# Kernel tuning notes

Measured on AMD Instinct MI355X. Metric: run time of the kernel, lower is better.

The kernel has to match this reference:

```python
import jax, jax.numpy as jnp
import numpy as np

B, H, W, C = 16, 48, 48, 256
D_INNER = 2 * C          # ssm_ratio = 2.0
D_STATE = 1
DT_RANK = C // 16        # mamba convention: dt_rank = d_model // 16
HID = 4 * C              # mlp_ratio = 4.0
N = H * W


def _grid_neighbors(h, w):
    idx = np.arange(h * w).reshape(h, w)
    pad_r = -np.ones((1, w), np.int64)
    pad_c = -np.ones((h, 1), np.int64)
    up = np.concatenate([pad_r, idx[:-1]], 0)
    down = np.concatenate([idx[1:], pad_r], 0)
    left = np.concatenate([pad_c, idx[:, :-1]], 1)
    right = np.concatenate([idx[:, 1:], pad_c], 1)
    nb = np.stack([up, down, left, right], -1).reshape(h * w, 4)
    valid = nb >= 0
    return jnp.asarray(np.where(valid, nb, 0), np.int32), jnp.asarray(valid)

_NBR, _VALID = _grid_neighbors(H, W)


def _mst(x):
    """Input-adaptive MST (Prim) on the 4-connected pixel grid.
    Edge weight = exp(1 - cosine_similarity) between adjacent pixel features.
    Returns (order, par): Prim insertion order (a valid BFS-like topological order:
    every node's parent appears earlier) and parent node id per node."""
    b = x.shape[0]
    f = x.reshape(b, N, C)
    f = f / (jnp.linalg.norm(f, axis=-1, keepdims=True) + 1e-8)
    cos = jnp.einsum('bnc,bnkc->bnk', f, f[:, _NBR])          # (B,N,4)
    wgt = jnp.where(_VALID, jnp.exp(1.0 - cos), jnp.inf)

    def prim(wb):
        key = jnp.full((N,), jnp.inf, wb.dtype).at[0].set(0.0)
        par = jnp.zeros((N,), jnp.int32)
        intree = jnp.zeros((N,), bool)

        def step(carry, _):
            key, par, intree = carry
            u = jnp.argmin(jnp.where(intree, jnp.inf, key)).astype(jnp.int32)
            intree = intree.at[u].set(True)
            nb, wv = _NBR[u], wb[u]
            better = (~intree[nb]) & (wv < key[nb])
            key = key.at[nb].set(jnp.where(better, wv, key[nb]))
            par = par.at[nb].set(jnp.where(better, u, par[nb]))
            return (key, par, intree), u

        (_, par, _), order = jax.lax.scan(step, (key, par, intree), None, length=N)
        return order, par

    return jax.vmap(prim)(wgt)


def _ln(x, g, b):
    m = jnp.mean(x, -1, keepdims=True)
    v = jnp.var(x, -1, keepdims=True)
    return (x - m) * jax.lax.rsqrt(v + 1e-5) * g + b


def _tree_ssm(xn, order, par, W_in, b_in, W_xp, W_dt, b_dt, A_log, Dp, W_out, b_out):
    """Mamba-style selective scan generalized to a tree: the hidden state of node v
    recurses from its MST parent instead of the previous sequence position."""
    b = xn.shape[0]
    xf = xn.reshape(b, N, C)
    xz = xf @ W_in + b_in                               # (B,N,2*D_INNER)
    xi, z = xz[..., :D_INNER], xz[..., D_INNER:]
    xi = jax.nn.silu(xi)
    dbc = xi @ W_xp                                     # (B,N,DT_RANK+2)
    dtr = dbc[..., :DT_RANK]
    Bv = dbc[..., DT_RANK:DT_RANK + 1]                  # d_state = 1
    Cv = dbc[..., DT_RANK + 1:DT_RANK + 2]
    dt = jax.nn.softplus(dtr @ W_dt + b_dt)             # (B,N,D_INNER)
    A = -jnp.exp(A_log)                                 # (D_INNER,)
    decay = jnp.exp(dt * A)
    Bx = dt * Bv * xi

    def tree_scan(ob, pb, db, xb):
        def step(hbuf, v):
            hv = db[v] * hbuf[pb[v]] + xb[v]            # h[v] = decay*h[parent] + B*x
            return hbuf.at[v].set(hv), None
        hbuf, _ = jax.lax.scan(step, jnp.zeros((N, D_INNER), db.dtype), ob)
        return hbuf

    h = jax.vmap(tree_scan)(order, par, decay, Bx)      # (B,N,D_INNER)
    y = Cv * h + Dp * xi
    return ((y * jax.nn.silu(z)) @ W_out + b_out).reshape(xn.shape)


def setup_inputs():
    key = jax.random.key(0)
    ks = jax.random.split(key, 8)
    g = lambda k, shp, s=0.02: jax.random.normal(k, shp, jnp.float32) * s
    return {
        "x": jax.random.normal(ks[0], (B, H, W, C), jnp.float32),
        "norm1_w": jnp.ones((C,), jnp.float32), "norm1_b": jnp.zeros((C,), jnp.float32),
        "norm2_w": jnp.ones((C,), jnp.float32), "norm2_b": jnp.zeros((C,), jnp.float32),
        "W_in": g(ks[1], (C, 2 * D_INNER)), "b_in": jnp.zeros((2 * D_INNER,), jnp.float32),
        "W_xp": g(ks[2], (D_INNER, DT_RANK + 2 * D_STATE)),
        "W_dt": g(ks[3], (DT_RANK, D_INNER), 0.1), "b_dt": jnp.full((D_INNER,), -2.0, jnp.float32),
        "A_log": jnp.zeros((D_INNER,), jnp.float32), "Dp": jnp.ones((D_INNER,), jnp.float32),
        "W_out": g(ks[4], (D_INNER, C)), "b_out": jnp.zeros((C,), jnp.float32),
        "fc1_w": g(ks[5], (C, HID)), "fc1_b": jnp.zeros((HID,), jnp.float32),
        "fc2_w": g(ks[6], (HID, C)), "fc2_b": jnp.zeros((C,), jnp.float32),
    }


def reference(x, norm1_w, norm1_b, norm2_w, norm2_b, W_in, b_in, W_xp, W_dt, b_dt,
              A_log, Dp, W_out, b_out, fc1_w, fc1_b, fc2_w, fc2_b):
    order, par = _mst(jax.lax.stop_gradient(x))         # torch.no_grad() MST
    x = x + _tree_ssm(_ln(x, norm1_w, norm1_b), order, par,
                      W_in, b_in, W_xp, W_dt, b_dt, A_log, Dp, W_out, b_out)
    h = jax.nn.gelu(_ln(x, norm2_w, norm2_b) @ fc1_w + fc1_b, approximate=False)
    return x + h @ fc2_w + fc2_b
```

## Files before the change

### kernel.cpp

```cpp
#include <hip/hip_runtime.h>
#include <math.h>

#define NN 2304
#define BB 16
#define CC 256
#define DI 512
#define MM (BB*NN)

typedef __attribute__((ext_vector_type(8))) short bf16x8;
typedef __attribute__((ext_vector_type(4))) float f32x4;

__device__ inline unsigned short f2b(float f){
  unsigned u = __float_as_uint(f);
  u = u + 0x7FFFu + ((u>>16)&1u);
  return (unsigned short)(u>>16);
}
__device__ inline float b2f(unsigned short s){ return __uint_as_float(((unsigned)s)<<16); }

__global__ __launch_bounds__(256) void k_wconv(const float* __restrict__ in, unsigned short* __restrict__ out, int R, int Ccols){
  int idx = blockIdx.x*256 + threadIdx.x;
  if (idx >= R*Ccols) return;
  int r = idx / Ccols, c = idx - r*Ccols;
  out[(size_t)c*R + r] = f2b(in[idx]);
}
__global__ __launch_bounds__(256) void k_t32(const float* __restrict__ in, float* __restrict__ out, int R, int Ccols){
  int idx = blockIdx.x*256 + threadIdx.x;
  if (idx >= R*Ccols) return;
  int r = idx / Ccols, c = idx - r*Ccols;
  out[(size_t)c*R + r] = in[idx];
}

__global__ __launch_bounds__(256) void k_norm(const float* __restrict__ x, float* __restrict__ innorm){
  int row = blockIdx.x*4 + (threadIdx.x>>6); int lane = threadIdx.x&63;
  float4 v = *(const float4*)(x + (size_t)row*CC + lane*4);
  float s = v.x*v.x + v.y*v.y + v.z*v.z + v.w*v.w;
  #pragma unroll
  for (int o=32;o;o>>=1) s += __shfl_xor(s,o);
  if (lane==0) innorm[row] = 1.0f/(sqrtf(s)+1e-8f);
}

__global__ __launch_bounds__(256) void k_edge(const float* __restrict__ x, const float* __restrict__ innorm, float* __restrict__ wgt){
  int g = blockIdx.x*4 + (threadIdx.x>>6); int lane = threadIdx.x&63;
  int b = g/NN, n = g - b*NN;
  int r = n/48, c = n - (n/48)*48;
  const float* xb = x + ((size_t)b*NN)*CC;
  float4 vu = *(const float4*)(xb + (size_t)n*CC + lane*4);
  int nb0=(r>0)?n-48:-1, nb1=(r<47)?n+48:-1, nb2=(c>0)?n-1:-1, nb3=(c<47)?n+1:-1;
  float d0=0,d1=0,d2=0,d3=0;
  if (nb0>=0){ float4 t=*(const float4*)(xb+(size_t)nb0*CC+lane*4); d0=vu.x*t.x+vu.y*t.y+vu.z*t.z+vu.w*t.w; }
  if (nb1>=0){ float4 t=*(const float4*)(xb+(size_t)nb1*CC+lane*4); d1=vu.x*t.x+vu.y*t.y+vu.z*t.z+vu.w*t.w; }
  if (nb2>=0){ float4 t=*(const float4*)(xb+(size_t)nb2*CC+lane*4); d2=vu.x*t.x+vu.y*t.y+vu.z*t.z+vu.w*t.w; }
  if (nb3>=0){ float4 t=*(const float4*)(xb+(size_t)nb3*CC+lane*4); d3=vu.x*t.x+vu.y*t.y+vu.z*t.z+vu.w*t.w; }
  #pragma unroll
  for (int o=32;o;o>>=1){ d0+=__shfl_xor(d0,o); d1+=__shfl_xor(d1,o); d2+=__shfl_xor(d2,o); d3+=__shfl_xor(d3,o); }
  if (lane==0){
    float inu = innorm[g];
    float inf_ = __uint_as_float(0x7F800000u);
    float4 w;
    w.x = (nb0>=0)? expf(1.0f - d0*(inu*innorm[g-n+nb0])) : inf_;
    w.y = (nb1>=0)? expf(1.0f - d1*(inu*innorm[g-n+nb1])) : inf_;
    w.z = (nb2>=0)? expf(1.0f - d2*(inu*innorm[g-n+nb2])) : inf_;
    w.w = (nb3>=0)? expf(1.0f - d3*(inu*innorm[g-n+nb3])) : inf_;
    *(float4*)(wgt + (size_t)g*4) = w;
  }
}

#define INFB 0x7F800000u
__device__ void mst_body(unsigned char* smem, const float* __restrict__ wgt, int b,
    unsigned short* __restrict__ parpos_g, int* __restrict__ lvlorder,
    int* __restrict__ lvlstart, int* __restrict__ nlvl)
{
  unsigned* comp   = (unsigned*)smem;
  unsigned* bestw  = (unsigned*)(smem + 9216);
  unsigned* bestid = (unsigned*)(smem + 18432);
  unsigned* tmask  = (unsigned*)(smem + 27648);
  unsigned* parpd  = (unsigned*)(smem + 36864);
  unsigned short* fr0 = (unsigned short*)(smem + 46080);
  unsigned short* fr1 = (unsigned short*)(smem + 50688);
  int* ctr = (int*)(smem + 55296);
  const int tid = threadIdx.x;
  const float* wb = wgt + (size_t)b*NN*4;

  #pragma unroll
  for (int k=0;k<9;k++){ int v=tid+k*256; comp[v]=v; tmask[v]=0u; }
  __syncthreads();

  for (int round=0; round<14; round++){
    #pragma unroll
    for (int k=0;k<9;k++){ int v=tid+k*256; bestw[v]=INFB; bestid[v]=0xFFFFFFFFu; }
    __syncthreads();
    unsigned candw[9], candi[9];
    #pragma unroll
    for (int k=0;k<9;k++){
      int v=tid+k*256;
      unsigned cv=comp[v];
      int r=v/48, c=v-(v/48)*48;
      float4 w4 = *(const float4*)(wb + (size_t)v*4);
      unsigned cw=INFB, ci=0xFFFFFFFFu;
      if (r>0  && comp[v-48]!=cv){ unsigned wv=__float_as_uint(w4.x); if (wv<cw){cw=wv;ci=(unsigned)(v*4+0);} }
      if (r<47 && comp[v+48]!=cv){ unsigned wv=__float_as_uint(w4.y); if (wv<cw){cw=wv;ci=(unsigned)(v*4+1);} }
      if (c>0  && comp[v-1] !=cv){ unsigned wv=__float_as_uint(w4.z); if (wv<cw){cw=wv;ci=(unsigned)(v*4+2);} }
      if (c<47 && comp[v+1] !=cv){ unsigned wv=__float_as_uint(w4.w); if (wv<cw){cw=wv;ci=(unsigned)(v*4+3);} }
      candw[k]=cw; candi[k]=ci;
      if (cw!=INFB) atomicMin(&bestw[cv], cw);
    }
    __syncthreads();
    #pragma unroll
    for (int k=0;k<9;k++){
      if (candw[k]!=INFB){
        int v=tid+k*256; unsigned cv=comp[v];
        if (bestw[cv]==candw[k]) atomicMin(&bestid[cv], candi[k]);
      }
    }
    __syncthreads();
    unsigned hookS[9];
    #pragma unroll
    for (int k=0;k<9;k++){
      int v=tid+k*256; hookS[k]=0xFFFFFFFFu;
      if (comp[v]!=(unsigned)v) continue;
      unsigned id=bestid[v];
      if (id==0xFFFFFFFFu) continue;
      int u=(int)(id>>2), d=(int)(id&3);
      int o = u + ((d==0)?-48:(d==1)?48:(d==2)?-1:1);
      unsigned s = comp[o];
      unsigned sid = bestid[s];
      bool mutual=false;
      if (sid!=0xFFFFFFFFu){
        int su=(int)(sid>>2), sd=(int)(sid&3);
        int so = su + ((sd==0)?-48:(sd==1)?48:(sd==2)?-1:1);
        mutual = (comp[so]==(unsigned)v);
      }
      if (!mutual || (unsigned)v>s) hookS[k]=s;
    }
    __syncthreads();
    #pragma unroll
    for (int k=0;k<9;k++){
      if (hookS[k]==0xFFFFFFFFu) continue;
      int v=tid+k*256;
      unsigned id=bestid[v];
      int u=(int)(id>>2), d=(int)(id&3);
      int o = u + ((d==0)?-48:(d==1)?48:(d==2)?-1:1);
      comp[v]=hookS[k];
      atomicOr(&tmask[u], 1u<<d);
      atomicOr(&tmask[o], 1u<<(d^1));
    }
    __syncthreads();
    for (int it=0; it<16; it++){
      if (tid==0) ctr[1]=0;
      __syncthreads();
      int ch=0;
      #pragma unroll
      for (int k=0;k<9;k++){
        int v=tid+k*256;
        unsigned c1=comp[v], c2=comp[c1];
        if (c1!=c2){ comp[v]=c2; ch=1; }
      }
      if (ch) atomicAdd(&ctr[1],1);
      __syncthreads();
      if (ctr[1]==0) break;
    }
    if (tid==0) ctr[2]=0;
    __syncthreads();
    int rc=0;
    #pragma unroll
    for (int k=0;k<9;k++){ int v=tid+k*256; if (comp[v]==(unsigned)v) rc++; }
    if (rc) atomicAdd(&ctr[2], rc);
    __syncthreads();
    if (ctr[2]<=1) break;
  }
  #pragma unroll
  for (int k=0;k<9;k++){ int v=tid+k*256; parpd[v]=0xFFFFFFFFu; }
  __syncthreads();
  if (tid >= 64) return;

  volatile unsigned* vpar = parpd;
  volatile int* vctr = ctr;
  volatile unsigned short* vf0 = fr0;
  volatile unsigned short* vf1 = fr1;
  if (tid==0){
    vpar[0]=0u; vf0[0]=0;
    lvlstart[b*(NN+2)+0]=0;
    lvlorder[b*NN+0]=0;
    parpos_g[b*NN+0]=0;
  }
  __builtin_amdgcn_wave_barrier();
  __builtin_amdgcn_sched_barrier(0);
  int lvl=0, base=0, cnt=1;
  volatile unsigned short* frA=vf0;
  volatile unsigned short* frB=vf1;
  while (true){
    if (tid==0) vctr[0]=0;
    __builtin_amdgcn_wave_barrier();
    __builtin_amdgcn_sched_barrier(0);
    for (int i=tid;i<cnt;i+=64){
      int v=(int)frA[i];
      unsigned m=tmask[v];
      int pv=(int)(vpar[v]&0xFFFFu);
      unsigned nv=((unsigned)(lvl+1)<<16)|(unsigned)v;
      #pragma unroll
      for (int d=0;d<4;d++){
        if ((m>>d)&1u){
          int nb = v + ((d==0)?-48:(d==1)?48:(d==2)?-1:1);
          if (nb!=pv && nb!=v){
            int pos=atomicAdd((int*)&ctr[0],1);
            vpar[nb]=nv;
            frB[pos]=(unsigned short)nb;
            lvlorder[b*NN + base + cnt + pos] = nb;
            parpos_g[b*NN + base + cnt + pos] = (unsigned short)(base + i);
          }
        }
      }
    }
    __builtin_amdgcn_wave_barrier();
    __builtin_amdgcn_sched_barrier(0);
    int ncnt=vctr[0];
    if (ncnt==0) break;
    if (tid==0) lvlstart[b*(NN+2)+(lvl+1)] = base+cnt;
    base+=cnt; cnt=ncnt; lvl++;
    volatile unsigned short* t=frA; frA=frB; frB=t;
    __builtin_amdgcn_wave_barrier();
    __builtin_amdgcn_sched_barrier(0);
  }
  if (tid==0){ nlvl[b]=lvl+1; lvlstart[b*(NN+2)+(lvl+1)]=base+cnt; }
}

template<int EPI>
__device__ void gemm_body(unsigned short* lA, unsigned short* lB, int bm, int bn,
    const unsigned short* __restrict__ A, const unsigned short* __restrict__ BT,
    const float* __restrict__ bias, int Ndim, int K,
    const float* __restrict__ addin, float* __restrict__ fout,
    unsigned short* __restrict__ bout0, unsigned short* __restrict__ bout1,
    const int* __restrict__ lvl)
{
  int tid=threadIdx.x, wid=tid>>6, lane=tid&63;
  const unsigned short* Ab = A + (size_t)bm*128*K;
  const unsigned short* Bb = BT + (size_t)bn*128*K;
  int wr=wid>>1, wc=wid&1;
  f32x4 acc[4][4];
  #pragma unroll
  for (int m2=0;m2<4;m2++)
    #pragma unroll
    for (int n2=0;n2<4;n2++)
      #pragma unroll
      for (int j=0;j<4;j++) acc[m2][n2][j]=0.f;
  int r0 = tid>>2, c0 = (tid&3)*8;
  for (int k0=0;k0<K;k0+=32){
    int4 va0 = *(const int4*)(Ab + (size_t)r0*K + k0 + c0);
    int4 va1 = *(const int4*)(Ab + (size_t)(r0+64)*K + k0 + c0);
    int4 vb0 = *(const int4*)(Bb + (size_t)r0*K + k0 + c0);
    int4 vb1 = *(const int4*)(Bb + (size_t)(r0+64)*K + k0 + c0);
    __syncthreads();
    *(int4*)(lA + r0*32 + c0) = va0;
    *(int4*)(lA + (r0+64)*32 + c0) = va1;
    *(int4*)(lB + r0*32 + c0) = vb0;
    *(int4*)(lB + (r0+64)*32 + c0) = vb1;
    __syncthreads();
    int ra = (wr<<6) + (lane&15);
    int rb = (wc<<6) + (lane&15);
    int cb = (lane>>4)<<3;
    bf16x8 af[4], bfr[4];
    #pragma unroll
    for (int m2=0;m2<4;m2++) af[m2] = *(const bf16x8*)(lA + (ra+m2*16)*32 + cb);
    #pragma unroll
    for (int n2=0;n2<4;n2++) bfr[n2] = *(const bf16x8*)(lB + (rb+n2*16)*32 + cb);
    #pragma unroll
    for (int m2=0;m2<4;m2++)
      #pragma unroll
      for (int n2=0;n2<4;n2++)
        acc[m2][n2] = __builtin_amdgcn_mfma_f32_16x16x32_bf16(af[m2], bfr[n2], acc[m2][n2], 0,0,0);
  }
  int rr = (lane>>4)<<2, cc = lane&15;
  #pragma unroll
  for (int m2=0;m2<4;m2++){
    #pragma unroll
    for (int n2=0;n2<4;n2++){
      int col = (bn<<7) + (wc<<6) + (n2<<4) + cc;
      float bs = bias[col];
      #pragma unroll
      for (int j=0;j<4;j++){
        int row = (bm<<7) + (wr<<6) + (m2<<4) + rr + j;
        float v = acc[m2][n2][j] + bs;
        if (EPI==0){
          float sv = v * (1.0f/(1.0f+expf(-v)));
          if (col < DI) bout0[(size_t)row*DI + col] = f2b(sv);
          else          bout1[(size_t)row*DI + col - DI] = f2b(sv);
        } else if (EPI==1){
          size_t oi=(size_t)row*Ndim+col;
          fout[oi] = addin[oi] + v;
        } else if (EPI==2){
          size_t oi=(size_t)row*Ndim+col;
          bout0[oi] = f2b(0.5f*v*(1.0f+erff(v*0.70710678118f)));
        } else if (EPI==3){
          int grow = (row/NN)*NN + lvl[row];
          fout[(size_t)row*Ndim+col] = addin[(size_t)grow*Ndim+col] + v;
        } else {
          int grow = (row/NN)*NN + lvl[row];
          fout[(size_t)grow*Ndim+col] = addin[(size_t)row*Ndim+col] + v;
        }
      }
    }
  }
}

template<int EPI>
__global__ __launch_bounds__(256) void k_gemm(
    const unsigned short* __restrict__ A, const unsigned short* __restrict__ BT,
    const float* __restrict__ bias, int Ndim, int K,
    const float* __restrict__ addin, float* __restrict__ fout,
    unsigned short* __restrict__ bout0, unsigned short* __restrict__ bout1,
    const int* __restrict__ lvl)
{
  __shared__ __align__(16) unsigned short lAB[128*32*2];
  int ntn = Ndim>>7;
  int bm = blockIdx.x/ntn, bn = blockIdx.x - bm*ntn;
  gemm_body<EPI>(lAB, lAB+128*32, bm, bn, A, BT, bias, Ndim, K, addin, fout, bout0, bout1, lvl);
}

__global__ __launch_bounds__(256) void k_fused(
    const unsigned short* __restrict__ xn, const unsigned short* __restrict__ WinT,
    const float* __restrict__ b_in,
    unsigned short* __restrict__ xi_b, unsigned short* __restrict__ sz_b,
    const float* __restrict__ wgt, unsigned short* __restrict__ parpos_g,
    int* __restrict__ lvlorder, int* __restrict__ lvlstart, int* __restrict__ nlvl)
{
  __shared__ __align__(16) unsigned char smem[55424];
  if (blockIdx.x < BB){
    mst_body(smem, wgt, blockIdx.x, parpos_g, lvlorder, lvlstart, nlvl);
  } else {
    int bid = blockIdx.x - BB;
    int bm = bid>>3, bn = bid&7;
    gemm_body<0>((unsigned short*)smem, (unsigned short*)smem + 128*32, bm, bn,
                 xn, WinT, b_in, 1024, 256, nullptr, nullptr, xi_b, sz_b, nullptr);
  }
}

__global__ __launch_bounds__(256) void k_ln(const float* __restrict__ xin, const float* __restrict__ g,
    const float* __restrict__ bta, unsigned short* __restrict__ outb)
{
  int row = blockIdx.x*4 + (threadIdx.x>>6); int lane=threadIdx.x&63;
  float4 v = *(const float4*)(xin + (size_t)row*CC + lane*4);
  float s = v.x+v.y+v.z+v.w;
  #pragma unroll
  for (int o=32;o;o>>=1) s += __shfl_xor(s,o);
  float m = s*(1.0f/256.0f);
  float dx=v.x-m, dy=v.y-m, dz=v.z-m, dw=v.w-m;
  float ss=dx*dx+dy*dy+dz*dz+dw*dw;
  #pragma unroll
  for (int o=32;o;o>>=1) ss += __shfl_xor(ss,o);
  float rs = rsqrtf(ss*(1.0f/256.0f)+1e-5f);
  int cb=lane*4;
  unsigned o0 = (unsigned)f2b(dx*rs*g[cb+0]+bta[cb+0]) | ((unsigned)f2b(dy*rs*g[cb+1]+bta[cb+1])<<16);
  unsigned o1 = (unsigned)f2b(dz*rs*g[cb+2]+bta[cb+2]) | ((unsigned)f2b(dw*rs*g[cb+3]+bta[cb+3])<<16);
  *(uint2*)(outb + (size_t)row*CC + cb) = make_uint2(o0,o1);
}

__global__ __launch_bounds__(256) void k_dbc(const unsigned short* __restrict__ xi_b,
    const float* __restrict__ WxpT, float* __restrict__ dbc)
{
  int row = blockIdx.x*4 + (threadIdx.x>>6); int lane=threadIdx.x&63;
  int4 raw = *(const int4*)(xi_b + (size_t)row*DI + lane*8);
  float xf[8];
  xf[0]=b2f((unsigned short)((unsigned)raw.x&0xFFFFu)); xf[1]=b2f((unsigned short)((unsigned)raw.x>>16));
  xf[2]=b2f((unsigned short)((unsigned)raw.y&0xFFFFu)); xf[3]=b2f((unsigned short)((unsigned)raw.y>>16));
  xf[4]=b2f((unsigned short)((unsigned)raw.z&0xFFFFu)); xf[5]=b2f((unsigned short)((unsigned)raw.z>>16));
  xf[6]=b2f((unsigned short)((unsigned)raw.w&0xFFFFu)); xf[7]=b2f((unsigned short)((unsigned)raw.w>>16));
  for (int jc=0;jc<18;jc++){
    const float* wr_ = WxpT + (size_t)jc*DI + lane*8;
    float s=0.f;
    #pragma unroll
    for (int t=0;t<8;t++) s += xf[t]*wr_[t];
    #pragma unroll
    for (int o=32;o;o>>=1) s += __shfl_xor(s,o);
    if (lane==0) dbc[(size_t)row*18+jc]=s;
  }
}

__global__ __launch_bounds__(512) void k_dbx(const float* __restrict__ dbc, const unsigned short* __restrict__ xi_b,
  const float* __restrict__ W_dt, const float* __restrict__ b_dt, const float* __restrict__ A_log,
  const int* __restrict__ lvlorder,
  unsigned short* __restrict__ dec_cm, unsigned short* __restrict__ bx_cm)
{
  __shared__ int smap[32];
  __shared__ float sd[32][18];
  int c = threadIdx.x;
  int b = blockIdx.x/72, pg = blockIdx.x - b*72;
  int p0 = pg*32;
  if (c<32) smap[c] = b*NN + lvlorder[b*NN + p0 + c];
  __syncthreads();
  for (int i=c;i<32*18;i+=512){ int rr=i/18, q=i-rr*18; sd[rr][q]=dbc[(size_t)smap[rr]*18+q]; }
  __syncthreads();
  float wdt[16];
  #pragma unroll
  for (int r2=0;r2<16;r2++) wdt[r2]=W_dt[r2*DI+c];
  float bd=b_dt[c];
  float nA=-expf(A_log[c]);
  unsigned decp[16], bxp[16];
  #pragma unroll
  for (int rr=0;rr<32;rr++){
    float a=bd;
    #pragma unroll
    for (int r2=0;r2<16;r2++) a += sd[rr][r2]*wdt[r2];
    float dt = (a>20.f)? a : log1pf(expf(a));
    float dec = expf(dt*nA);
    float bx = dt*sd[rr][16]*b2f(xi_b[(size_t)smap[rr]*DI + c]);
    if (rr&1){ decp[rr>>1] |= ((unsigned)f2b(dec))<<16; bxp[rr>>1] |= ((unsigned)f2b(bx))<<16; }
    else     { decp[rr>>1]  =  (unsigned)f2b(dec);      bxp[rr>>1]  =  (unsigned)f2b(bx); }
  }
  size_t chb = ((size_t)b*DI + c)*NN + p0;
  uint4* dp = (uint4*)(dec_cm + chb);
  uint4* bp = (uint4*)(bx_cm + chb);
  #pragma unroll
  for (int q=0;q<4;q++){
    uint4 dv, bv;
    dv.x=decp[q*4+0]; dv.y=decp[q*4+1]; dv.z=decp[q*4+2]; dv.w=decp[q*4+3];
    bv.x=bxp[q*4+0];  bv.y=bxp[q*4+1];  bv.z=bxp[q*4+2];  bv.w=bxp[q*4+3];
    dp[q]=dv; bp[q]=bv;
  }
}

#define SCH 4
__global__ __launch_bounds__(256) void k_scan(const unsigned short* __restrict__ dec_cm,
    unsigned short* __restrict__ bx_cm,
    const unsigned short* __restrict__ parpos_g,
    const int* __restrict__ lvlstart, const int* __restrict__ nlvl)
{
  __shared__ unsigned short sdec[SCH*NN];
  __shared__ unsigned short sbx[SCH*NN];
  __shared__ unsigned short spp[NN];
  int b = blockIdx.x>>7, t = blockIdx.x&127;
  int c0 = t*SCH;
  int tid = threadIdx.x;
  const size_t gch = ((size_t)b*DI + c0)*NN;
  #pragma unroll
  for (int cc=0;cc<SCH;cc++){
    const uint2* gd = (const uint2*)(dec_cm + gch + (size_t)cc*NN);
    const uint2* gb = (const uint2*)(bx_cm + gch + (size_t)cc*NN);
    uint2* ld = (uint2*)(sdec + cc*NN);
    uint2* lb = (uint2*)(sbx + cc*NN);
    for (int i=tid;i<NN/4;i+=256){ ld[i]=gd[i]; lb[i]=gb[i]; }
  }
  for (int i=tid;i<NN;i+=256) spp[i]=parpos_g[b*NN+i];
  int nlv = nlvl[b];
  __syncthreads();
  for (int lvl=1; lvl<nlv; lvl++){
    int s=lvlstart[b*(NN+2)+lvl], e=lvlstart[b*(NN+2)+lvl+1];
    int tot=(e-s)*SCH;
    for (int idx=tid; idx<tot; idx+=256){
      int p = s + (idx>>2);
      int cc = idx&3;
      int pp = spp[p];
      float hv = b2f(sdec[cc*NN+p])*b2f(sbx[cc*NN+pp]) + b2f(sbx[cc*NN+p]);
      sbx[cc*NN+p] = f2b(hv);
    }
    __syncthreads();
  }
  #pragma unroll
  for (int cc=0;cc<SCH;cc++){
    uint2* gb = (uint2*)(bx_cm + gch + (size_t)cc*NN);
    const uint2* lb = (const uint2*)(sbx + cc*NN);
    for (int i=tid;i<NN/4;i+=256) gb[i]=lb[i];
  }
}

__global__ __launch_bounds__(512) void k_u(const unsigned short* __restrict__ h_cm,
    const unsigned short* __restrict__ xi_b, const unsigned short* __restrict__ sz_b,
    const float* __restrict__ dbc, const float* __restrict__ Dp,
    const int* __restrict__ lvlorder, unsigned short* __restrict__ u_perm)
{
  __shared__ int smap[32];
  __shared__ unsigned short hT[32*512];
  int c = threadIdx.x;
  int b = blockIdx.x/72, pg = blockIdx.x - b*72;
  int p0 = pg*32;
  if (c<32) smap[c] = b*NN + lvlorder[b*NN + p0 + c];
  {
    const uint4* gh = (const uint4*)(h_cm + ((size_t)b*DI + c)*NN + p0);
    #pragma unroll
    for (int q=0;q<4;q++){
      uint4 w = gh[q];
      unsigned ws[4] = {w.x,w.y,w.z,w.w};
      #pragma unroll
      for (int e=0;e<4;e++){
        hT[(q*8+e*2+0)*512 + c] = (unsigned short)(ws[e]&0xFFFFu);
        hT[(q*8+e*2+1)*512 + c] = (unsigned short)(ws[e]>>16);
      }
    }
  }
  float dpc = Dp[c];
  __syncthreads();
  #pragma unroll 4
  for (int rr=0;rr<32;rr++){
    int grow = smap[rr];
    float Cv = dbc[(size_t)grow*18+17];
    float xiv = b2f(xi_b[(size_t)grow*DI + c]);
    float szv = b2f(sz_b[(size_t)grow*DI + c]);
    float hv = b2f(hT[rr*512 + c]);
    float u = (Cv*hv + dpc*xiv)*szv;
    u_perm[((size_t)(b*NN + p0 + rr))*DI + c] = f2b(u);
  }
}

extern "C" void kernel_launch(void* const* d_in, const int* in_sizes, int n_in,
                              void* d_out, int out_size, void* d_ws, size_t ws_size,
                              hipStream_t stream) {
  (void)in_sizes; (void)n_in; (void)out_size; (void)ws_size;
  const float* x      = (const float*)d_in[0];
  const float* n1w    = (const float*)d_in[1];
  const float* n1b    = (const float*)d_in[2];
  const float* n2w    = (const float*)d_in[3];
  const float* n2b    = (const float*)d_in[4];
  const float* W_in   = (const float*)d_in[5];
  const float* b_in   = (const float*)d_in[6];
  const float* W_xp   = (const float*)d_in[7];
  const float* W_dt   = (const float*)d_in[8];
  const float* b_dt   = (const float*)d_in[9];
  const float* A_log  = (const float*)d_in[10];
  const float* Dp     = (const float*)d_in[11];
  const float* W_out  = (const float*)d_in[12];
  const float* b_out  = (const float*)d_in[13];
  const float* fc1_w  = (const float*)d_in[14];
  const float* fc1_b  = (const float*)d_in[15];
  const float* fc2_w  = (const float*)d_in[16];
  const float* fc2_b  = (const float*)d_in[17];

  char* base=(char*)d_ws; size_t off=0;
  auto alc=[&](size_t nb)->char*{ char* p=base+off; off=(off+nb+255)&~(size_t)255; return p; };
  float* wgt            = (float*)alc((size_t)MM*4*4);
  float* innorm         = (float*)alc((size_t)MM*4);
  unsigned short* parpos= (unsigned short*)alc((size_t)MM*2);
  int* lvlorder         = (int*)alc((size_t)MM*4);
  int* lvlstart         = (int*)alc((size_t)BB*(NN+2)*4);
  int* nlvl             = (int*)alc((size_t)BB*4);
  unsigned short* xi_b  = (unsigned short*)alc((size_t)MM*DI*2);
  unsigned short* sz_b  = (unsigned short*)alc((size_t)MM*DI*2);
  float* dbc            = (float*)alc((size_t)MM*18*4);
  unsigned short* dec_cm= (unsigned short*)alc((size_t)MM*DI*2);
  unsigned short* bx_cm = (unsigned short*)alc((size_t)MM*DI*2);
  unsigned short* WinT  = (unsigned short*)alc((size_t)CC*1024*2);
  unsigned short* WoutT = (unsigned short*)alc((size_t)DI*CC*2);
  unsigned short* fc1T  = (unsigned short*)alc((size_t)CC*1024*2);
  unsigned short* fc2T  = (unsigned short*)alc((size_t)1024*CC*2);
  float* WxpT           = (float*)alc((size_t)DI*18*4);
  unsigned short* xn      = (unsigned short*)dec_cm;
  unsigned short* h_cm    = bx_cm;
  unsigned short* u_perm  = dec_cm;
  float* x2_perm          = (float*)bx_cm;
  unsigned short* x2n_perm= dec_cm;
  unsigned short* g1_perm = xi_b;

  k_wconv<<<dim3((256*1024+255)/256),dim3(256),0,stream>>>(W_in, WinT, 256,1024);
  k_wconv<<<dim3((512*256 +255)/256),dim3(256),0,stream>>>(W_out, WoutT, 512,256);
  k_wconv<<<dim3((256*1024+255)/256),dim3(256),0,stream>>>(fc1_w, fc1T, 256,1024);
  k_wconv<<<dim3((1024*256+255)/256),dim3(256),0,stream>>>(fc2_w, fc2T, 1024,256);
  k_t32  <<<dim3((512*18  +255)/256),dim3(256),0,stream>>>(W_xp, WxpT, 512,18);

  k_norm<<<dim3(MM/4),dim3(256),0,stream>>>(x, innorm);
  k_edge<<<dim3(MM/4),dim3(256),0,stream>>>(x, innorm, wgt);
  k_ln<<<dim3(MM/4),dim3(256),0,stream>>>(x, n1w, n1b, xn);

  k_fused<<<dim3(BB + 288*8),dim3(256),0,stream>>>(xn, WinT, b_in, xi_b, sz_b,
                                                   wgt, parpos, lvlorder, lvlstart, nlvl);

  k_dbc<<<dim3(MM/4),dim3(256),0,stream>>>(xi_b, WxpT, dbc);
  k_dbx<<<dim3(MM/32),dim3(512),0,stream>>>(dbc, xi_b, W_dt, b_dt, A_log, lvlorder, dec_cm, bx_cm);
  k_scan<<<dim3(BB*128),dim3(256),0,stream>>>(dec_cm, bx_cm, parpos, lvlstart, nlvl);
  k_u<<<dim3(MM/32),dim3(512),0,stream>>>(h_cm, xi_b, sz_b, dbc, Dp, lvlorder, u_perm);

  k_gemm<3><<<dim3(288*2),dim3(256),0,stream>>>(u_perm, WoutT, b_out, 256, 512,
                                                x, x2_perm, nullptr, nullptr, lvlorder);
  k_ln<<<dim3(MM/4),dim3(256),0,stream>>>(x2_perm, n2w, n2b, x2n_perm);
  k_gemm<2><<<dim3(288*8),dim3(256),0,stream>>>(x2n_perm, fc1T, fc1_b, 1024, 256,
                                                nullptr, nullptr, g1_perm, nullptr, nullptr);
  k_gemm<4><<<dim3(288*2),dim3(256),0,stream>>>(g1_perm, fc2T, fc2_b, 256, 1024,
                                                x2_perm, (float*)d_out, nullptr, nullptr, lvlorder);
}
```

Before: 871.5 us.

## Replace serial single-wave BFS leveling with Euler-tour pointer-jumping depth computation

After the Boruvka MST, the per-batch tree leveling used a single 64-thread wave doing a frontier BFS, one level at a time with atomics. That step is replaced by an Euler tour over directed tree edges, ranked with two pointer-jumping passes across all 256 threads. The first pass orients edges to find parents, the second computes signed prefix sums to get depths. Levels are then bucketed with a shared-memory histogram and prefix scan. This removes the serial per-level loop, whose length depends on tree depth, at the cost of more shared memory (which lowers occupancy for the co-scheduled GEMM blocks) and fixed iteration counts of 13 jumps.

```diff
diff --git a/kernel.cpp b/kernel.cpp
--- a/kernel.cpp
+++ b/kernel.cpp
@@ -16,6 +16,7 @@
   return (unsigned short)(u>>16);
 }
 __device__ inline float b2f(unsigned short s){ return __uint_as_float(((unsigned)s)<<16); }
+__device__ __forceinline__ int dstep(int d){ return (d==0)?-48:(d==1)?48:(d==2)?-1:1; }
 
 __global__ __launch_bounds__(256) void k_wconv(const float* __restrict__ in, unsigned short* __restrict__ out, int R, int Ccols){
   int idx = blockIdx.x*256 + threadIdx.x;
@@ -66,18 +67,20 @@
 }
 
 #define INFB 0x7F800000u
+#define NILA 0x3FFFu
 __device__ void mst_body(unsigned char* smem, const float* __restrict__ wgt, int b,
     unsigned short* __restrict__ parpos_g, int* __restrict__ lvlorder,
     int* __restrict__ lvlstart, int* __restrict__ nlvl)
 {
-  unsigned* comp   = (unsigned*)smem;
-  unsigned* bestw  = (unsigned*)(smem + 9216);
-  unsigned* bestid = (unsigned*)(smem + 18432);
-  unsigned* tmask  = (unsigned*)(smem + 27648);
-  unsigned* parpd  = (unsigned*)(smem + 36864);
-  unsigned short* fr0 = (unsigned short*)(smem + 46080);
-  unsigned short* fr1 = (unsigned short*)(smem + 50688);
-  int* ctr = (int*)(smem + 55296);
+  unsigned* tmask = (unsigned*)smem;
+  unsigned* pk    = (unsigned*)(smem + 9216);
+  unsigned* comp   = pk;
+  unsigned* bestw  = pk + 2304;
+  unsigned* bestid = pk + 4608;
+  unsigned short* par   = (unsigned short*)(smem + 46080);
+  unsigned short* dpos  = (unsigned short*)(smem + 50688);
+  int* hist = (int*)(smem + 55296);
+  int* ctr  = (int*)(smem + 64512);
   const int tid = threadIdx.x;
   const float* wb = wgt + (size_t)b*NN*4;
 
@@ -121,13 +124,13 @@
       unsigned id=bestid[v];
       if (id==0xFFFFFFFFu) continue;
       int u=(int)(id>>2), d=(int)(id&3);
-      int o = u + ((d==0)?-48:(d==1)?48:(d==2)?-1:1);
+      int o = u + dstep(d);
       unsigned s = comp[o];
       unsigned sid = bestid[s];
       bool mutual=false;
       if (sid!=0xFFFFFFFFu){
         int su=(int)(sid>>2), sd=(int)(sid&3);
-        int so = su + ((sd==0)?-48:(sd==1)?48:(sd==2)?-1:1);
+        int so = su + dstep(sd);
         mutual = (comp[so]==(unsigned)v);
       }
       if (!mutual || (unsigned)v>s) hookS[k]=s;
@@ -139,7 +142,7 @@
       int v=tid+k*256;
       unsigned id=bestid[v];
       int u=(int)(id>>2), d=(int)(id&3);
-      int o = u + ((d==0)?-48:(d==1)?48:(d==2)?-1:1);
+      int o = u + dstep(d);
       comp[v]=hookS[k];
       atomicOr(&tmask[u], 1u<<d);
       atomicOr(&tmask[o], 1u<<(d^1));
@@ -168,60 +171,103 @@
     __syncthreads();
     if (ctr[2]<=1) break;
   }
-  #pragma unroll
-  for (int k=0;k<9;k++){ int v=tid+k*256; parpd[v]=0xFFFFFFFFu; }
-  __syncthreads();
-  if (tid >= 64) return;
-
-  volatile unsigned* vpar = parpd;
-  volatile int* vctr = ctr;
-  volatile unsigned short* vf0 = fr0;
-  volatile unsigned short* vf1 = fr1;
-  if (tid==0){
-    vpar[0]=0u; vf0[0]=0;
-    lvlstart[b*(NN+2)+0]=0;
-    lvlorder[b*NN+0]=0;
-    parpos_g[b*NN+0]=0;
-  }
-  __builtin_amdgcn_wave_barrier();
-  __builtin_amdgcn_sched_barrier(0);
-  int lvl=0, base=0, cnt=1;
-  volatile unsigned short* frA=vf0;
-  volatile unsigned short* frB=vf1;
-  while (true){
-    if (tid==0) vctr[0]=0;
-    __builtin_amdgcn_wave_barrier();
-    __builtin_amdgcn_sched_barrier(0);
-    for (int i=tid;i<cnt;i+=64){
-      int v=(int)frA[i];
-      unsigned m=tmask[v];
-      int pv=(int)(vpar[v]&0xFFFFu);
-      unsigned nv=((unsigned)(lvl+1)<<16)|(unsigned)v;
+  __syncthreads();
+
+  int a0;
+  { unsigned m0 = tmask[0]; a0 = __ffs((int)(m0&0xFu))-1; }
+
+  for (int pass=0; pass<2; pass++){
+    for (int k=0;k<36;k++){
+      int a = k*256+tid;
+      int v = a>>2, d = a&3;
+      unsigned mv = tmask[v];
+      unsigned sc = NILA;
+      unsigned vl = pass ? 8192u : 0u;
+      if ((mv>>d)&1u){
+        int w = v + dstep(d);
+        unsigned mw = tmask[w];
+        int rd = d^1;
+        int nd = -1;
+        #pragma unroll
+        for (int kk=1;kk<=4;kk++){ int c2=(rd+kk)&3; if (nd<0 && ((mw>>c2)&1u)) nd=c2; }
+        sc = (unsigned)(w*4+nd);
+        if (sc==(unsigned)a0) sc=NILA;
+        vl = pass ? (8192u + (((mv>>(4+d))&1u)? 1u : (unsigned)-1)) : 1u;
+      }
+      pk[a] = (sc<<14) | (vl & 0x3FFFu);
+    }
+    __syncthreads();
+    for (int it=0; it<13; it++){
+      unsigned stg[36];
       #pragma unroll
-      for (int d=0;d<4;d++){
-        if ((m>>d)&1u){
-          int nb = v + ((d==0)?-48:(d==1)?48:(d==2)?-1:1);
-          if (nb!=pv && nb!=v){
-            int pos=atomicAdd((int*)&ctr[0],1);
-            vpar[nb]=nv;
-            frB[pos]=(unsigned short)nb;
-            lvlorder[b*NN + base + cnt + pos] = nb;
-            parpos_g[b*NN + base + cnt + pos] = (unsigned short)(base + i);
+      for (int k=0;k<36;k++){
+        int a=k*256+tid;
+        unsigned mine=pk[a];
+        unsigned s=mine>>14;
+        if (s==NILA) stg[k]=mine;
+        else {
+          unsigned oth=pk[s];
+          unsigned nv=(mine&0x3FFFu)+(oth&0x3FFFu);
+          if (pass) nv -= 8192u;
+          stg[k]=((oth>>14)<<14)|(nv&0x3FFFu);
+        }
+      }
+      __syncthreads();
+      #pragma unroll
+      for (int k=0;k<36;k++) pk[k*256+tid]=stg[k];
+      __syncthreads();
+    }
+    if (pass==0){
+      for (int k=0;k<36;k++){
+        int a=k*256+tid;
+        int v=a>>2, d=a&3;
+        if ((tmask[v]>>d)&1u){
+          int w=v+dstep(d);
+          int ra=w*4+(d^1);
+          if ((pk[a]&0x3FFFu) > (pk[ra]&0x3FFFu)){
+            atomicOr(&tmask[v], 16u<<d);
+            par[w]=(unsigned short)v;
           }
         }
       }
-    }
-    __builtin_amdgcn_wave_barrier();
-    __builtin_amdgcn_sched_barrier(0);
-    int ncnt=vctr[0];
-    if (ncnt==0) break;
-    if (tid==0) lvlstart[b*(NN+2)+(lvl+1)] = base+cnt;
-    base+=cnt; cnt=ncnt; lvl++;
-    volatile unsigned short* t=frA; frA=frB; frB=t;
-    __builtin_amdgcn_wave_barrier();
-    __builtin_amdgcn_sched_barrier(0);
-  }
-  if (tid==0){ nlvl[b]=lvl+1; lvlstart[b*(NN+2)+(lvl+1)]=base+cnt; }
+      __syncthreads();
+    }
+  }
+  if (tid==0){ par[0]=0; dpos[0]=0; ctr[3]=0; }
+  __syncthreads();
+  for (int k=0;k<36;k++){
+    int a=k*256+tid;
+    int v=a>>2, d=a&3;
+    unsigned mv=tmask[v];
+    if (((mv>>d)&1u) && ((mv>>(4+d))&1u)){
+      int w=v+dstep(d);
+      int S=(int)(pk[a]&0x3FFFu)-8192;
+      int dep=1-S;
+      dpos[w]=(unsigned short)dep;
+      atomicMax(&ctr[3],dep);
+    }
+  }
+  __syncthreads();
+  int nlv_=ctr[3]+1;
+  for (int i=tid;i<nlv_;i+=256) hist[i]=0;
+  __syncthreads();
+  for (int i=tid;i<NN;i+=256) atomicAdd(&hist[dpos[i]],1);
+  __syncthreads();
+  if (tid==0){
+    int run=0;
+    for (int l=0;l<nlv_;l++){ int c2=hist[l]; hist[l]=run; lvlstart[b*(NN+2)+l]=run; run+=c2; }
+    lvlstart[b*(NN+2)+nlv_]=run;
+    nlvl[b]=nlv_;
+  }
+  __syncthreads();
+  for (int i=tid;i<NN;i+=256){
+    int pos=atomicAdd(&hist[dpos[i]],1);
+    lvlorder[b*NN+pos]=i;
+    dpos[i]=(unsigned short)pos;
+  }
+  __syncthreads();
+  for (int i=tid;i<NN;i+=256)
+    parpos_g[b*NN + dpos[i]] = dpos[par[i]];
 }
 
 template<int EPI>
@@ -323,7 +369,7 @@
     const float* __restrict__ wgt, unsigned short* __restrict__ parpos_g,
     int* __restrict__ lvlorder, int* __restrict__ lvlstart, int* __restrict__ nlvl)
 {
-  __shared__ __align__(16) unsigned char smem[55424];
+  __shared__ __align__(16) unsigned char smem[64528];
   if (blockIdx.x < BB){
     mst_body(smem, wgt, blockIdx.x, parpos_g, lvlorder, lvlstart, nlvl);
   } else {
```

New measurement: 729.7 us. 16.3% less time.
